# Optimization experiments

Measured on AMD Instinct MI355X. Metric: run time of the kernel, lower is better.

The kernel has to match this reference:

```python
import math
import jax, jax.numpy as jnp
import numpy as np

NUM_HEADS = 16
D_MODEL = 1024
WINDOW = 512


def alibi_slopes(num_heads):
    # 1 / ((2**8)**((i+1)/num_heads))  for i in range(num_heads)
    x = (2.0 ** 8) ** (1.0 / num_heads)
    return jnp.asarray([1.0 / x ** (i + 1) for i in range(num_heads)], dtype=jnp.float32)


def setup_inputs() -> dict:
    key = jax.random.key(0)
    k1, k2 = jax.random.split(key)
    x = jax.random.normal(k1, (1, 4096, D_MODEL), dtype=jnp.float32)
    # scale weight like a trained init so softmax isn't saturated
    w_kqv = jax.random.normal(k2, (D_MODEL, 3 * D_MODEL), dtype=jnp.float32) * 0.02
    return {"x": x, "w_kqv": w_kqv}


def reference(x, w_kqv):
    B, S, D = x.shape
    H = NUM_HEADS
    hd = D // H
    scale = math.sqrt(D)  # module scales by sqrt(d_model), not sqrt(head_dim)

    kqv = x @ w_kqv                       # [B, S, 3D]
    k, q, v = jnp.split(kqv, 3, axis=-1)  # chunk order: key, query, value
    k = k.reshape(B, S, H, hd).transpose(0, 2, 1, 3)  # [B, H, S, hd]
    q = q.reshape(B, S, H, hd).transpose(0, 2, 1, 3)
    v = v.reshape(B, S, H, hd).transpose(0, 2, 1, 3)

    # ALiBi bias: m_h * (j - i)
    pos = jnp.arange(S)
    rel = pos[None, :] - pos[:, None]                  # [S, S] = x - y
    bias = alibi_slopes(H)[:, None, None] * rel.astype(jnp.float32)  # [H, S, S]

    score = jnp.einsum("bhqd,bhkd->bhqk", q, k) / scale + bias[None]

    # causal sliding-window mask: allow 0 <= i - j <= WINDOW
    dist = pos[:, None] - pos[None, :]                 # i - j
    mask = (dist >= 0) & (dist <= WINDOW)              # [S, S]
    score = jnp.where(mask[None, None], score, -jnp.inf)

    attn = jax.nn.softmax(score, axis=-1)
    out = jnp.einsum("bhqk,bhkd->bhqd", attn, v)       # [B, H, S, hd]
    out = out.transpose(0, 2, 1, 3).reshape(B, S, D)
    return out
```

## Files before the change

kernel.cpp:

```cpp
#include <hip/hip_runtime.h>
#include <hip/hip_bf16.h>

#define SEQ   4096
#define DM    1024
#define NH    16
#define HD    64
#define N3    3072
#define WIN   512

#define LOG2E 1.4426950408889634f

typedef __attribute__((ext_vector_type(8))) short short8;
typedef __attribute__((ext_vector_type(4))) short short4v;
typedef __attribute__((ext_vector_type(4))) float float4v;

__device__ __forceinline__ float bf16_bits_to_float(unsigned short u) {
  return __uint_as_float(((unsigned int)u) << 16);
}

typedef __attribute__((address_space(3))) void lds_void_t;
typedef __attribute__((address_space(1))) const void gbl_void_t;
__device__ __forceinline__ void async_copy16(void* lds_dst, const void* g_src) {
  __builtin_amdgcn_global_load_lds((gbl_void_t*)g_src, (lds_void_t*)lds_dst,
                                   16, 0, 0);
}

template <int NT>
__device__ __forceinline__ int detect_fp32(const unsigned short* __restrict__ probe,
                                           float* red) {
  const int t = threadIdx.x;
  float mx = 0.0f;
#pragma unroll
  for (int p = 0; p < 8; ++p) {
    float v = bf16_bits_to_float(probe[(t * 8 + p) * 2]);
    if (v != v) v = 1e38f;
    mx = fmaxf(mx, fabsf(v));
  }
  red[t] = mx;
  __syncthreads();
  for (int s = NT / 2; s > 0; s >>= 1) {
    if (t < s) red[t] = fmaxf(red[t], red[t + s]);
    __syncthreads();
  }
  const int fl = red[0] > 100.0f ? 1 : 0;
  __syncthreads();
  return fl;
}

__device__ __forceinline__ int detect_fp32_wave(
    const unsigned short* __restrict__ probe) {
  const int lane = threadIdx.x & 63;
  float mx = 0.0f;
#pragma unroll
  for (int p = 0; p < 8; ++p) {
    float v = bf16_bits_to_float(probe[(lane * 8 + p) * 2]);
    if (v != v) v = 1e38f;
    mx = fmaxf(mx, fabsf(v));
  }
  return __any(mx > 100.0f) ? 1 : 0;
}

__global__ __launch_bounds__(256) void prep(
    const void* __restrict__ x, const void* __restrict__ w,
    __hip_bfloat16* __restrict__ xb, __hip_bfloat16* __restrict__ wt) {
  __shared__ __hip_bfloat16 tile[64][66];
  __shared__ float red[256];
  const int t = threadIdx.x;
  if (blockIdx.x < 2048) {
    const int fl = detect_fp32<256>((const unsigned short*)x, red);
    const int i0 = (blockIdx.x * 256 + t) * 8;
    if (fl) {
      const float* xf = (const float*)x + i0;
      float4 f0 = *(const float4*)(xf);
      float4 f1 = *(const float4*)(xf + 4);
      __hip_bfloat16 tmp[8];
      tmp[0] = __float2bfloat16(f0.x); tmp[1] = __float2bfloat16(f0.y);
      tmp[2] = __float2bfloat16(f0.z); tmp[3] = __float2bfloat16(f0.w);
      tmp[4] = __float2bfloat16(f1.x); tmp[5] = __float2bfloat16(f1.y);
      tmp[6] = __float2bfloat16(f1.z); tmp[7] = __float2bfloat16(f1.w);
      *(uint4*)&xb[i0] = *(const uint4*)tmp;
    } else {
      *(uint4*)&xb[i0] = *(const uint4*)((const __hip_bfloat16*)x + i0);
    }
  } else {
    const int bid = blockIdx.x - 2048;
    const int fl = detect_fp32<256>((const unsigned short*)w, red);
    const int n0 = (bid % 48) * 64;
    const int k0 = (bid / 48) * 64;
    const int tx = t & 63, ty0 = t >> 6;
    if (fl) {
      const float* wf = (const float*)w;
#pragma unroll
      for (int p = 0; p < 16; ++p) {
        int row = ty0 + p * 4;
        tile[row][tx] = __float2bfloat16(wf[(k0 + row) * N3 + n0 + tx]);
      }
    } else {
      const __hip_bfloat16* wb = (const __hip_bfloat16*)w;
#pragma unroll
      for (int p = 0; p < 16; ++p) {
        int row = ty0 + p * 4;
        tile[row][tx] = wb[(k0 + row) * N3 + n0 + tx];
      }
    }
    __syncthreads();
#pragma unroll
    for (int r = 0; r < 2; ++r) {
      int oe = r * 2048 + t * 8;
      int nr = oe >> 6, kc = oe & 63;
      __hip_bfloat16 v[8];
#pragma unroll
      for (int e = 0; e < 8; ++e) v[e] = tile[kc + e][nr];
      *(uint4*)&wt[(n0 + nr) * DM + k0 + kc] = *(const uint4*)v;
    }
  }
}

__global__ __launch_bounds__(256) void gemm_kqv(
    const __hip_bfloat16* __restrict__ A,
    const __hip_bfloat16* __restrict__ BT,
    __hip_bfloat16* __restrict__ C) {
  __shared__ __align__(16) __hip_bfloat16 As[2][128 * 32];
  __shared__ __align__(16) __hip_bfloat16 Bs[2][128 * 32];
  const int m0 = blockIdx.y * 128;
  const int n0 = blockIdx.x * 128;
  const int t = threadIdx.x;
  const int wave = t >> 6, lane = t & 63;
  const int wm = wave >> 1, wn = wave & 1;
  const int l15 = lane & 15, quad = lane >> 4;

  const int srow0 = wave * 16 + (lane >> 2);
  const int scol  = (lane & 3) * 8;
  const int sbyte = wave * 1024 + lane * 16;

  float4v acc[4][4] = {};

  for (int k0 = 0; k0 < DM; k0 += 64) {
    __syncthreads();
#pragma unroll
    for (int half = 0; half < 2; ++half) {
      const int kk = k0 + half * 32;
#pragma unroll
      for (int r = 0; r < 2; ++r) {
        const int row = srow0 + r * 64;
        async_copy16((char*)As[half] + r * 4096 + sbyte,
                     &A[(m0 + row) * DM + kk + scol]);
        async_copy16((char*)Bs[half] + r * 4096 + sbyte,
                     &BT[(n0 + row) * DM + kk + scol]);
      }
    }
    __syncthreads();

#pragma unroll
    for (int half = 0; half < 2; ++half) {
      short8 a[4], b[4];
#pragma unroll
      for (int mi = 0; mi < 4; ++mi)
        a[mi] = *(const short8*)(&As[half][(wm * 64 + mi * 16 + l15) * 32 + quad * 8]);
#pragma unroll
      for (int ni = 0; ni < 4; ++ni)
        b[ni] = *(const short8*)(&Bs[half][(wn * 64 + ni * 16 + l15) * 32 + quad * 8]);
#pragma unroll
      for (int mi = 0; mi < 4; ++mi)
#pragma unroll
        for (int ni = 0; ni < 4; ++ni)
          acc[mi][ni] = __builtin_amdgcn_mfma_f32_16x16x32_bf16(
              a[mi], b[ni], acc[mi][ni], 0, 0, 0);
    }
  }

#pragma unroll
  for (int mi = 0; mi < 4; ++mi)
#pragma unroll
    for (int ni = 0; ni < 4; ++ni)
#pragma unroll
      for (int r = 0; r < 4; ++r) {
        int row = m0 + wm * 64 + mi * 16 + quad * 4 + r;
        int col = n0 + wn * 64 + ni * 16 + l15;
        C[row * N3 + col] = __float2bfloat16(acc[mi][ni][r]);
      }
}

__global__ __launch_bounds__(256, 4) void attn(
    const __hip_bfloat16* __restrict__ kqv,
    const unsigned short* __restrict__ xprobe,
    void* __restrict__ out) {
  __shared__ __align__(16) __hip_bfloat16 Ks[64 * 72];
  __shared__ __align__(16) __hip_bfloat16 Vt[80 * 68];
  __shared__ __align__(16) __hip_bfloat16 Ps[64 * 72];

  const int fl = detect_fp32_wave(xprobe);
  const int h  = blockIdx.y;
  const int bx = blockIdx.x;
  const int i0 = 64 * ((bx & 7) * 8 + (bx >> 3));
  const int t    = threadIdx.x;
  const int wave = t >> 6, lane = t & 63;
  const int l15 = lane & 15, quad = lane >> 4;
  const float slope2  = exp2f(-0.5f * (float)(h + 1)) * LOG2E;
  const float nslope2 = -slope2;
  const float qscale  = LOG2E / 32.0f;

  for (int idx = t; idx < 16 * 68; idx += 256) {
    int rr = idx / 68, cc = idx - rr * 68;
    ((unsigned short*)Vt)[(64 + rr) * 68 + cc] = (rr == 0) ? 0x3F80 : 0;
  }

  short8 aq[2];
#pragma unroll
  for (int ks2 = 0; ks2 < 2; ++ks2)
    aq[ks2] = *(const short8*)&kqv[(i0 + wave * 16 + l15) * N3 + DM + h * HD +
                                   ks2 * 32 + quad * 8];

  float4v o[5] = {};

  const int jlo  = max(0, i0 - WIN);
  const int nblk = (i0 + 64 - jlo) >> 6;

  const int krow0 = t >> 3, krow1 = (t >> 3) + 32, kd0 = (t & 7) * 8;
  const int vr0 = (t >> 3) * 2, vd0 = (t & 7) * 8;
  uint4 kregA, kregB, vregA, vregB;
  kregA = *(const uint4*)&kqv[(jlo + krow0) * N3 + h * HD + kd0];
  kregB = *(const uint4*)&kqv[(jlo + krow1) * N3 + h * HD + kd0];
  vregA = *(const uint4*)&kqv[(jlo + vr0) * N3 + 2 * DM + h * HD + vd0];
  vregB = *(const uint4*)&kqv[(jlo + vr0 + 1) * N3 + 2 * DM + h * HD + vd0];

  for (int b = 0; b < nblk; ++b) {
    const int j0 = jlo + b * 64;
    __syncthreads();
    *(uint4*)&Ks[krow0 * 72 + kd0] = kregA;
    *(uint4*)&Ks[krow1 * 72 + kd0] = kregB;
    {
      const unsigned short* pa = (const unsigned short*)&vregA;
      const unsigned short* pb = (const unsigned short*)&vregB;
#pragma unroll
      for (int e = 0; e < 8; ++e) {
        unsigned int pack = (unsigned int)pa[e] | ((unsigned int)pb[e] << 16);
        *(unsigned int*)&Vt[(vd0 + e) * 68 + vr0] = pack;
      }
    }
    __syncthreads();

    if (b + 1 < nblk) {
      const int jn = j0 + 64;
      kregA = *(const uint4*)&kqv[(jn + krow0) * N3 + h * HD + kd0];
      kregB = *(const uint4*)&kqv[(jn + krow1) * N3 + h * HD + kd0];
      vregA = *(const uint4*)&kqv[(jn + vr0) * N3 + 2 * DM + h * HD + vd0];
      vregB = *(const uint4*)&kqv[(jn + vr0 + 1) * N3 + 2 * DM + h * HD + vd0];
    }

    float4v sacc[4] = {};
#pragma unroll
    for (int ks2 = 0; ks2 < 2; ++ks2)
#pragma unroll
      for (int nt = 0; nt < 4; ++nt) {
        short8 bk = *(const short8*)&Ks[(nt * 16 + l15) * 72 + ks2 * 32 + quad * 8];
        sacc[nt] = __builtin_amdgcn_mfma_f32_16x16x32_bf16(aq[ks2], bk, sacc[nt], 0, 0, 0);
      }

    const int dbase = (i0 + wave * 16 + quad * 4) - (j0 + l15);
    const float s16 = nslope2 * -16.0f;
#pragma unroll
    for (int r = 0; r < 4; ++r) {
      float bias = nslope2 * (float)(dbase + r);
      int rel = dbase + r;
#pragma unroll
      for (int nt = 0; nt < 4; ++nt) {
        float x = fmaf(sacc[nt][r], qscale, bias);
        x = ((unsigned)rel <= (unsigned)WIN) ? x : -200.0f;
        Ps[(wave * 16 + quad * 4 + r) * 72 + nt * 16 + l15] =
            __float2bfloat16(exp2f(x));
        bias += s16;
        rel -= 16;
      }
    }

#pragma unroll
    for (int ks = 0; ks < 64; ks += 32) {
      short8 ap = *(const short8*)&Ps[(wave * 16 + l15) * 72 + ks + quad * 8];
#pragma unroll
      for (int dt = 0; dt < 5; ++dt) {
        const __hip_bfloat16* vp = &Vt[(dt * 16 + l15) * 68 + ks + quad * 8];
        short4v v0 = *(const short4v*)vp;
        short4v v1 = *(const short4v*)(vp + 4);
        short8 bv = __builtin_shufflevector(v0, v1, 0, 1, 2, 3, 4, 5, 6, 7);
        o[dt] = __builtin_amdgcn_mfma_f32_16x16x32_bf16(ap, bv, o[dt], 0, 0, 0);
      }
    }
  }

#pragma unroll
  for (int r = 0; r < 4; ++r) {
    const float l = __shfl(o[4][r], quad * 16, 64);
    const float inv_l = 1.0f / l;
    const int row = i0 + wave * 16 + quad * 4 + r;
#pragma unroll
    for (int dt = 0; dt < 4; ++dt) {
      const int idx = row * DM + h * HD + dt * 16 + l15;
      const float v = o[dt][r] * inv_l;
      if (fl) ((float*)out)[idx] = v;
      else    ((__hip_bfloat16*)out)[idx] = __float2bfloat16(v);
    }
  }
}

extern "C" void kernel_launch(void* const* d_in, const int* in_sizes, int n_in,
                              void* d_out, int out_size, void* d_ws, size_t ws_size,
                              hipStream_t stream) {
  char* ws = (char*)d_ws;
  __hip_bfloat16* wt  = (__hip_bfloat16*)(ws + 4096);
  __hip_bfloat16* kqv = (__hip_bfloat16*)(ws + 4096 + 6291456);
  __hip_bfloat16* xb  = (__hip_bfloat16*)d_out;

  hipLaunchKernelGGL(prep, dim3(2048 + 768), dim3(256), 0, stream,
                     d_in[0], d_in[1], xb, wt);
  hipLaunchKernelGGL(gemm_kqv, dim3(24, 32), dim3(256), 0, stream, xb, wt, kqv);
  hipLaunchKernelGGL(attn, dim3(64, 16), dim3(256), 0, stream,
                     kqv, (const unsigned short*)d_in[0], d_out);
}
```

Before: 147.4 us.

## Swizzle transposed V tile in LDS and vectorize P stores via key permutation

The transposed V tile moves to a 72-element row stride with an XOR swizzle keyed on the row group. The PV MFMA can then read each B operand with a single 128-bit LDS load instead of two 64-bit loads, and bank conflicts on those reads are meant to drop. The key order inside each 64-key block is permuted consistently in V and P, so each lane writes its four probabilities as one packed short4 store instead of four scalar bf16 stores. The cost is more index arithmetic, and correctness now depends on the V-load row mapping, the swizzle and the P column permutation all staying in agreement.

```diff
diff --git a/kernel.cpp b/kernel.cpp
--- a/kernel.cpp
+++ b/kernel.cpp
@@ -186,7 +186,7 @@
     const unsigned short* __restrict__ xprobe,
     void* __restrict__ out) {
   __shared__ __align__(16) __hip_bfloat16 Ks[64 * 72];
-  __shared__ __align__(16) __hip_bfloat16 Vt[80 * 68];
+  __shared__ __align__(16) __hip_bfloat16 Vt[80 * 72];
   __shared__ __align__(16) __hip_bfloat16 Ps[64 * 72];
 
   const int fl = detect_fp32_wave(xprobe);
@@ -200,9 +200,9 @@
   const float nslope2 = -slope2;
   const float qscale  = LOG2E / 32.0f;
 
-  for (int idx = t; idx < 16 * 68; idx += 256) {
-    int rr = idx / 68, cc = idx - rr * 68;
-    ((unsigned short*)Vt)[(64 + rr) * 68 + cc] = (rr == 0) ? 0x3F80 : 0;
+  for (int idx = t; idx < 16 * 64; idx += 256) {
+    int rr = idx >> 6, cc = idx & 63;
+    ((unsigned short*)Vt)[(64 + rr) * 72 + cc] = (rr == 0) ? 0x3F80 : 0;
   }
 
   short8 aq[2];
@@ -217,12 +217,16 @@
   const int nblk = (i0 + 64 - jlo) >> 6;
 
   const int krow0 = t >> 3, krow1 = (t >> 3) + 32, kd0 = (t & 7) * 8;
-  const int vr0 = (t >> 3) * 2, vd0 = (t & 7) * 8;
+  const int rbase = t >> 3;
+  const int vd0   = (t & 7) * 8;
+  const int kA    = (rbase & 15) + ((rbase >> 4) << 5);
+  const int vsig2 = (((rbase & 15) << 2) + ((rbase >> 4) << 1)) * 2;
+  const int vswz  = (t & 7) << 4;
   uint4 kregA, kregB, vregA, vregB;
   kregA = *(const uint4*)&kqv[(jlo + krow0) * N3 + h * HD + kd0];
   kregB = *(const uint4*)&kqv[(jlo + krow1) * N3 + h * HD + kd0];
-  vregA = *(const uint4*)&kqv[(jlo + vr0) * N3 + 2 * DM + h * HD + vd0];
-  vregB = *(const uint4*)&kqv[(jlo + vr0 + 1) * N3 + 2 * DM + h * HD + vd0];
+  vregA = *(const uint4*)&kqv[(jlo + kA) * N3 + 2 * DM + h * HD + vd0];
+  vregB = *(const uint4*)&kqv[(jlo + kA + 16) * N3 + 2 * DM + h * HD + vd0];
 
   for (int b = 0; b < nblk; ++b) {
     const int j0 = jlo + b * 64;
@@ -232,10 +236,11 @@
     {
       const unsigned short* pa = (const unsigned short*)&vregA;
       const unsigned short* pb = (const unsigned short*)&vregB;
+      char* vbase = (char*)Vt;
 #pragma unroll
       for (int e = 0; e < 8; ++e) {
         unsigned int pack = (unsigned int)pa[e] | ((unsigned int)pb[e] << 16);
-        *(unsigned int*)&Vt[(vd0 + e) * 68 + vr0] = pack;
+        *(unsigned int*)(vbase + (vd0 + e) * 144 + (vsig2 ^ vswz)) = pack;
       }
     }
     __syncthreads();
@@ -244,8 +249,8 @@
       const int jn = j0 + 64;
       kregA = *(const uint4*)&kqv[(jn + krow0) * N3 + h * HD + kd0];
       kregB = *(const uint4*)&kqv[(jn + krow1) * N3 + h * HD + kd0];
-      vregA = *(const uint4*)&kqv[(jn + vr0) * N3 + 2 * DM + h * HD + vd0];
-      vregB = *(const uint4*)&kqv[(jn + vr0 + 1) * N3 + 2 * DM + h * HD + vd0];
+      vregA = *(const uint4*)&kqv[(jn + kA) * N3 + 2 * DM + h * HD + vd0];
+      vregB = *(const uint4*)&kqv[(jn + kA + 16) * N3 + 2 * DM + h * HD + vd0];
     }
 
     float4v sacc[4] = {};
@@ -259,19 +264,22 @@
 
     const int dbase = (i0 + wave * 16 + quad * 4) - (j0 + l15);
     const float s16 = nslope2 * -16.0f;
+    const int psbase = (wave * 16 + quad * 4) * 72 + l15 * 4;
 #pragma unroll
     for (int r = 0; r < 4; ++r) {
       float bias = nslope2 * (float)(dbase + r);
       int rel = dbase + r;
+      short4v pk;
 #pragma unroll
       for (int nt = 0; nt < 4; ++nt) {
         float x = fmaf(sacc[nt][r], qscale, bias);
         x = ((unsigned)rel <= (unsigned)WIN) ? x : -200.0f;
-        Ps[(wave * 16 + quad * 4 + r) * 72 + nt * 16 + l15] =
-            __float2bfloat16(exp2f(x));
+        __hip_bfloat16 hb = __float2bfloat16(exp2f(x));
+        pk[nt] = *reinterpret_cast<const short*>(&hb);
         bias += s16;
         rel -= 16;
       }
+      *(short4v*)&Ps[psbase + r * 72] = pk;
     }
 
 #pragma unroll
@@ -279,10 +287,9 @@
       short8 ap = *(const short8*)&Ps[(wave * 16 + l15) * 72 + ks + quad * 8];
 #pragma unroll
       for (int dt = 0; dt < 5; ++dt) {
-        const __hip_bfloat16* vp = &Vt[(dt * 16 + l15) * 68 + ks + quad * 8];
-        short4v v0 = *(const short4v*)vp;
-        short4v v1 = *(const short4v*)(vp + 4);
-        short8 bv = __builtin_shufflevector(v0, v1, 0, 1, 2, 3, 4, 5, 6, 7);
+        const int vrow = dt * 16 + l15;
+        const short8 bv = *(const short8*)((const char*)Vt + vrow * 144 +
+            ((ks * 2 + (quad << 4)) ^ (((vrow >> 3) & 7) << 4)));
         o[dt] = __builtin_amdgcn_mfma_f32_16x16x32_bf16(ap, bv, o[dt], 0, 0, 0);
       }
     }
```

Result: no change. 148.5 us (+0.8%).
